# Optimization experiments

Measured on AMD Instinct MI355X. Metric: run time of the kernel, lower is better.

Reference implementation:

```python
import jax, jax.numpy as jnp
from jax import lax
import numpy as np

B, C, O, NF, H, W = 4, 64, 64, 64, 128, 128
DK = 3
K = DK * DK
PAD = DK // 2


def setup_inputs() -> dict:
    key = jax.random.key(0)
    k0, k1, k2, k3 = jax.random.split(key, 4)
    inputs = jax.random.normal(k0, (B, C, H, W), jnp.float32)
    feat = jax.random.normal(k1, (B, NF, H, W), jnp.float32)
    # small offset-conv weights keep learned offsets in a realistic sub-pixel range
    om_w = jax.random.normal(k2, (C * 3 * K, NF, 3, 3), jnp.float32) * 0.02
    om_b = jnp.zeros((C * 3 * K,), jnp.float32)
    dc_w = jax.random.normal(k3, (O, C, DK, DK), jnp.float32) * (1.0 / np.sqrt(C * K))
    dc_b = jnp.zeros((O,), jnp.float32)
    return dict(inputs=inputs, feat=feat, om_w=om_w, om_b=om_b, dc_w=dc_w, dc_b=dc_b)


def _gather(img, y, x):
    # img: [B,C,H,W]; y,x: int32 [B,C,K,H,W]; zero outside bounds
    valid = (y >= 0) & (y < H) & (x >= 0) & (x < W)
    yc = jnp.clip(y, 0, H - 1)
    xc = jnp.clip(x, 0, W - 1)
    idx = (yc * W + xc).reshape(B, C, K, H * W)
    flat = img.reshape(B, C, 1, H * W)
    v = jnp.take_along_axis(flat, idx, axis=3).reshape(B, C, K, H, W)
    return jnp.where(valid, v, 0.0)


def _forward(inputs, feat, om_w, om_b, dc_w, dc_b):
    # offset/mask conv: nf -> in_nc*3*K, 3x3, pad 1
    off_msk = lax.conv_general_dilated(
        feat, om_w, (1, 1), ((1, 1), (1, 1)),
        dimension_numbers=('NCHW', 'OIHW', 'NCHW')) + om_b[None, :, None, None]
    # offsets interleaved (y,x) per kernel tap per deformable group (= channel)
    off = off_msk[:, :C * 2 * K].reshape(B, C, K, 2, H, W)
    msk = jax.nn.sigmoid(off_msk[:, C * 2 * K:]).reshape(B, C, K, H, W)

    ky = (jnp.arange(K) // DK - PAD).astype(jnp.float32)  # [K]
    kx = (jnp.arange(K) % DK - PAD).astype(jnp.float32)
    hg = jnp.arange(H, dtype=jnp.float32)
    wg = jnp.arange(W, dtype=jnp.float32)
    py = hg[None, None, None, :, None] + ky[None, None, :, None, None] + off[:, :, :, 0]  # [B,C,K,H,W]
    px = wg[None, None, None, None, :] + kx[None, None, :, None, None] + off[:, :, :, 1]

    y0f = jnp.floor(py); x0f = jnp.floor(px)
    wy = py - y0f; wx = px - x0f
    y0 = y0f.astype(jnp.int32); x0 = x0f.astype(jnp.int32)
    y1 = y0 + 1; x1 = x0 + 1

    v00 = _gather(inputs, y0, x0)
    v01 = _gather(inputs, y0, x1)
    v10 = _gather(inputs, y1, x0)
    v11 = _gather(inputs, y1, x1)
    sampled = ((1 - wy) * (1 - wx) * v00 + (1 - wy) * wx * v01
               + wy * (1 - wx) * v10 + wy * wx * v11) * msk  # [B,C,K,H,W]

    out = jnp.einsum('bckhw,ock->bohw', sampled, dc_w.reshape(O, C, K))
    out = out + dc_b[None, :, None, None]
    return jax.nn.relu(out)


def reference(inputs, feat, om_w, om_b, dc_w, dc_b):
    return _forward(inputs, feat, om_w, om_b, dc_w, dc_b)
```

## Files before the change

### kernel.cpp

```cpp
#include <hip/hip_runtime.h>
#include <hip/hip_bf16.h>

typedef __bf16 bf16;
typedef __bf16 bf16x8 __attribute__((ext_vector_type(8)));
typedef __bf16 bf16x4 __attribute__((ext_vector_type(4)));
typedef float f32x4 __attribute__((ext_vector_type(4)));
typedef float f32x2 __attribute__((ext_vector_type(2)));
typedef float f32x2u __attribute__((ext_vector_type(2))) __attribute__((aligned(4)));
typedef int  i32x4 __attribute__((ext_vector_type(4)));

#define MFMA16(a, b, c) __builtin_amdgcn_mfma_f32_16x16x32_bf16((a), (b), (c), 0, 0, 0)

static constexpr size_t FEATS_OFF = 0;
static constexpr size_t OMW3_OFF  = 8388608;
static constexpr size_t DCW_OFF   = OMW3_OFF + 1990656;
static constexpr size_t SC_OFF    = DCW_OFF + 73728;
static constexpr size_t PAD_OFF   = SC_OFF + 9216;


__global__ void prep_featS(const float* __restrict__ feat, bf16* __restrict__ featS) {
    const int hh = blockIdx.x, b = blockIdx.y;
    __shared__ float t[64][129];
    for (int i = threadIdx.x; i < 64 * 32; i += 256) {
        int cf = i >> 5, q = i & 31;
        const float* src = feat + ((size_t)(b * 64 + cf) * 128 + hh) * 128 + q * 4;
        t[cf][q * 4 + 0] = src[0];
        t[cf][q * 4 + 1] = src[1];
        t[cf][q * 4 + 2] = src[2];
        t[cf][q * 4 + 3] = src[3];
    }
    __syncthreads();
    for (int i = threadIdx.x; i < 1024; i += 256) {
        int px = i >> 3, cfb = i & 7;
        int sb = cfb ^ (px & 7);
        bf16x8 v;
#pragma unroll
        for (int e = 0; e < 8; ++e) v[e] = (bf16)t[cfb * 8 + e][px];
        *(bf16x8*)(featS + ((size_t)((b * 128 + hh) * 128 + px) << 6) + sb * 8) = v;
    }
}

__global__ void prep_weights(const float* __restrict__ om_w, const float* __restrict__ om_b,
                             const float* __restrict__ dc_w,
                             bf16* __restrict__ omw3, bf16* __restrict__ dcw2p,
                             float* __restrict__ scf) {
    int i = blockIdx.x * 256 + threadIdx.x;
    if (i < 995328) {
        int e = i & 511, lane = e >> 3, j = e & 7;
        int q = i >> 9;
        int t = q % 3, q2 = q / 3, kk = q2 % 18, ct = q2 / 18;
        int ck = ct * 16 + (lane & 15);
        int kcol = kk * 32 + (lane >> 4) * 8 + j;
        int tap = kcol >> 6, cf = kcol & 63;
        int ch = (t < 2) ? (ck * 2 + t) : (1152 + ck);
        omw3[i] = (bf16)om_w[ch * 576 + cf * 9 + tap];
    }
    if (i < 36864) {
        int j = i & 7, lane = (i >> 3) & 63, ot = (i >> 9) & 3, win = i >> 11;
        int o = ot * 16 + (lane & 15);
        int ck = win * 32 + (lane >> 4) * 8 + j;
        dcw2p[i] = (bf16)dc_w[o * 576 + ck];
    }
    if (i < 576) {
        int ck = i;
        int c = ck / 9, kd = ck - 9 * c, kq = kd / 3, kx = kd - 3 * kq;
        int pr = ck >> 1, lo = ck & 1;
        scf[pr * 8 + 0 + lo] = om_b[ck * 2]     + (float)(kq + 2);
        scf[pr * 8 + 2 + lo] = om_b[ck * 2 + 1] + (float)(kx + 2);
        scf[pr * 8 + 4 + lo] = om_b[1152 + ck];
        scf[pr * 8 + 6 + lo] = __uint_as_float((unsigned)(c * 17956));
    }
}

__global__ void prep_pad(const float* __restrict__ inputs, float* __restrict__ pad) {
    int yy = blockIdx.x, bc = blockIdx.y, xx = threadIdx.x;
    if (xx >= 134) return;
    float v = 0.f;
    if (yy >= 3 && yy <= 130 && xx >= 3 && xx <= 130)
        v = inputs[(size_t)bc * 16384 + (yy - 3) * 128 + (xx - 3)];
    pad[((size_t)bc * 134 + yy) * 134 + xx] = v;
}


__global__ void __launch_bounds__(256, 4)
deform_fused(const float* __restrict__ pad,
             const bf16* __restrict__ featS,
             const bf16* __restrict__ omw3,
             const bf16* __restrict__ dcw2p,
             const f32x4* __restrict__ sconst,
             const float* __restrict__ dcb,
             float* __restrict__ out)
{
    const int bid = blockIdx.x;
    const int P0 = (bid & 1) << 6;
    const int h = (bid >> 1) & 127;
    const int b = bid >> 8;
    const int tid = threadIdx.x;
    const int lane = tid & 63;
    const int wid_s = __builtin_amdgcn_readfirstlane(tid >> 6);
    const int l15 = lane & 15, g = lane >> 4;

    __shared__ __align__(16) unsigned char smem[25344 + 8192];
    char* featB = (char*)smem;
    char* sampB = (char*)smem + 25344;

    for (int i = tid; i < 6336; i += 256) ((unsigned*)featB)[i] = 0u;
    __syncthreads();
    {
        const int s0 = (P0 == 0) ? 0 : 63;
        const int q0 = (P0 == 0) ? 1 : 0;
        for (int i = tid; i < 1560; i += 256) {
            int ky = i / 520, rem = i - ky * 520, row = rem >> 3, c = rem & 7;
            int hh = h - 1 + ky;
            if ((unsigned)hh < 128u) {
                const char* src = (const char*)featS
                    + (((size_t)(b * 128 + hh) * 128 + s0 + row) << 7) + c * 16;
                *(i32x4*)(featB + ((ky * 66 + q0 + row) << 7) + c * 16) = *(const i32x4*)src;
            }
        }
    }
    __syncthreads();

    int fb[18];
#pragma unroll
    for (int kk = 0; kk < 18; ++kk) {
        const int tap = kk >> 1;
        const int kyp = tap / 3, kxp = tap - 3 * kyp;
        const int q = l15 + kxp;
        fb[kk] = (kyp * 66 + q) * 128 + ((((kk & 1) * 4 + g) ^ ((q + 7) & 7)) << 4);
    }

    f32x4 acc2[4];
#pragma unroll
    for (int u = 0; u < 4; ++u) acc2[u] = (f32x4){0.f, 0.f, 0.f, 0.f};

    const bf16* omw3_l = omw3 + lane * 8;
    const bf16* dcw_l  = dcw2p + lane * 8;
    const float* padb0 = pad + (size_t)b * 64 * 17956;
    const f32x2 hb2 = {(float)h, (float)h};
    const f32x2 fx2 = {(float)(P0 + l15), (float)(P0 + l15)};
    const int g4 = g * 4;

#pragma unroll 1
    for (int blk = 0; blk < 9; ++blk) {
        f32x4 acc1[3][4];
#pragma unroll
        for (int t = 0; t < 3; ++t)
#pragma unroll
            for (int nf = 0; nf < 4; ++nf) acc1[t][nf] = (f32x4){0.f, 0.f, 0.f, 0.f};

        const int abase = (blk * 4 + wid_s) * 27648;

#pragma unroll
        for (int kk = 0; kk < 18; ++kk) {
            bf16x8 a0 = *(const bf16x8*)(omw3_l + abase + ((kk * 3 + 0) << 9));
            bf16x8 a1 = *(const bf16x8*)(omw3_l + abase + ((kk * 3 + 1) << 9));
            bf16x8 a2 = *(const bf16x8*)(omw3_l + abase + ((kk * 3 + 2) << 9));
            bf16x8 bfr[4];
#pragma unroll
            for (int nf = 0; nf < 4; ++nf)
                bfr[nf] = *(const bf16x8*)(featB + fb[kk] + nf * 2048);
            __builtin_amdgcn_s_setprio(1);
#pragma unroll
            for (int nf = 0; nf < 4; ++nf) {
                acc1[0][nf] = MFMA16(a0, bfr[nf], acc1[0][nf]);
                acc1[1][nf] = MFMA16(a1, bfr[nf], acc1[1][nf]);
                acc1[2][nf] = MFMA16(a2, bfr[nf], acc1[2][nf]);
            }
            __builtin_amdgcn_s_setprio(0);
        }

        bf16x8 aK0 = *(const bf16x8*)(dcw_l + ((blk * 8 + wid_s) << 9));
        bf16x8 aK1 = *(const bf16x8*)(dcw_l + ((blk * 8 + 4 + wid_s) << 9));

        const f32x4* scB = sconst + (blk * 64 + wid_s * 16);
        f32x4 e0A = scB[g4 + 0], e1A = scB[g4 + 1];
        f32x4 e0B = scB[g4 + 2], e1B = scB[g4 + 3];
        f32x2 yb[2], xb[2], mb[2];
        unsigned co[2][2];
        yb[0] = f32x2{e0A.x, e0A.y} + hb2;
        xb[0] = f32x2{e0A.z, e0A.w} + fx2;
        mb[0] = f32x2{e1A.x, e1A.y};
        co[0][0] = __float_as_uint(e1A.z); co[0][1] = __float_as_uint(e1A.w);
        yb[1] = f32x2{e0B.x, e0B.y} + hb2;
        xb[1] = f32x2{e0B.z, e0B.w} + fx2;
        mb[1] = f32x2{e1B.x, e1B.y};
        co[1][0] = __float_as_uint(e1B.z); co[1][1] = __float_as_uint(e1B.w);

#pragma unroll
        for (int nf = 0; nf < 4; ++nf) {
            float s[4];
#pragma unroll
            for (int pi = 0; pi < 2; ++pi) {
                f32x2 py = f32x2{acc1[0][nf][2 * pi], acc1[0][nf][2 * pi + 1]} + yb[pi];
                f32x2 px = f32x2{acc1[1][nf][2 * pi], acc1[1][nf][2 * pi + 1]} + xb[pi];
                f32x2 lg = f32x2{acc1[2][nf][2 * pi], acc1[2][nf][2 * pi + 1]} + mb[pi];
#pragma unroll
                for (int e = 0; e < 2; ++e) {
                    float pyc = __builtin_amdgcn_fmed3f(py[e], 0.5f, 132.5f);
                    float pxc = __builtin_amdgcn_fmed3f(px[e], 0.5f, 132.5f);
                    int y0 = (int)pyc, x0 = (int)pxc;
                    float wy = __builtin_amdgcn_fractf(pyc);
                    float wx = __builtin_amdgcn_fractf(pxc);
                    unsigned off = co[pi][e] + (unsigned)(y0 * 134 + x0);
                    f32x2u t0 = *(const f32x2u*)(padb0 + off);
                    f32x2u t1 = *(const f32x2u*)(padb0 + off + 134);
                    float top = t0.x + wx * (t0.y - t0.x);
                    float bot = t1.x + wx * (t1.y - t1.x);
                    float bil = top + wy * (bot - top);
                    float mk = __builtin_amdgcn_rcpf(1.f + __expf(-lg[e]));
                    s[2 * pi + e] = bil * mk;
                }
            }
            bf16x4 pk4 = {(bf16)s[0], (bf16)s[1], (bf16)s[2], (bf16)s[3]};
            *(bf16x4*)(sampB + (nf * 16 + l15) * 128
                       + (((wid_s * 4 + g) ^ ((l15 & 7) << 1)) << 3)) = pk4;
            xb[0] += 16.f; xb[1] += 16.f;
        }
        __syncthreads();

        const int rb_swz = (g ^ (l15 & 7)) << 4;
        __builtin_amdgcn_s_setprio(1);
#pragma unroll
        for (int u = 0; u < 4; ++u) {
            const int rb = (u * 16 + l15) * 128 + rb_swz;
            bf16x8 b0 = *(const bf16x8*)(sampB + rb);
            bf16x8 b1 = *(const bf16x8*)(sampB + (rb ^ 64));
            acc2[u] = MFMA16(aK0, b0, acc2[u]);
            acc2[u] = MFMA16(aK1, b1, acc2[u]);
        }
        __builtin_amdgcn_s_setprio(0);
        __syncthreads();
    }

    float bias[4];
#pragma unroll
    for (int r = 0; r < 4; ++r) bias[r] = dcb[wid_s * 16 + g * 4 + r];
#pragma unroll
    for (int u = 0; u < 4; ++u)
#pragma unroll
        for (int r = 0; r < 4; ++r) {
            int o = wid_s * 16 + g * 4 + r;
            out[((size_t)(b * 64 + o) * 128 + h) * 128 + P0 + u * 16 + l15]
                = fmaxf(acc2[u][r] + bias[r], 0.f);
        }
}

extern "C" void kernel_launch(void* const* d_in, const int* in_sizes, int n_in,
                              void* d_out, int out_size, void* d_ws, size_t ws_size,
                              hipStream_t stream) {
    const float* inputs = (const float*)d_in[0];
    const float* feat   = (const float*)d_in[1];
    const float* om_w   = (const float*)d_in[2];
    const float* om_b   = (const float*)d_in[3];
    const float* dc_w   = (const float*)d_in[4];
    const float* dc_b   = (const float*)d_in[5];
    float* out = (float*)d_out;

    char* ws = (char*)d_ws;
    bf16*  featS  = (bf16*)(ws + FEATS_OFF);
    bf16*  omw3   = (bf16*)(ws + OMW3_OFF);
    bf16*  dcw2p  = (bf16*)(ws + DCW_OFF);
    float* scf    = (float*)(ws + SC_OFF);
    float* pad    = (float*)(ws + PAD_OFF);

    prep_featS<<<dim3(128, 4), 256, 0, stream>>>(feat, featS);
    prep_weights<<<(995328 + 255) / 256, 256, 0, stream>>>(om_w, om_b, dc_w, omw3, dcw2p, scf);
    prep_pad<<<dim3(134, 256), 256, 0, stream>>>(inputs, pad);

    deform_fused<<<1024, 256, 0, stream>>>(pad, featS, omw3, dcw2p,
                                           (const f32x4*)scf, dc_b, out);
}
```

Measured before the change: 177.2 us.

## Switch fused deform kernel to 32x32x16 MFMA with register-resident samples

```diff
diff --git a/kernel.cpp b/kernel.cpp
--- a/kernel.cpp
+++ b/kernel.cpp
@@ -3,17 +3,16 @@
 
 typedef __bf16 bf16;
 typedef __bf16 bf16x8 __attribute__((ext_vector_type(8)));
-typedef __bf16 bf16x4 __attribute__((ext_vector_type(4)));
 typedef float f32x4 __attribute__((ext_vector_type(4)));
-typedef float f32x2 __attribute__((ext_vector_type(2)));
+typedef float f32x16 __attribute__((ext_vector_type(16)));
 typedef float f32x2u __attribute__((ext_vector_type(2))) __attribute__((aligned(4)));
 typedef int  i32x4 __attribute__((ext_vector_type(4)));
 
-#define MFMA16(a, b, c) __builtin_amdgcn_mfma_f32_16x16x32_bf16((a), (b), (c), 0, 0, 0)
+#define MFMA32(a, b, c) __builtin_amdgcn_mfma_f32_32x32x16_bf16((a), (b), (c), 0, 0, 0)
 
 static constexpr size_t FEATS_OFF = 0;
-static constexpr size_t OMW3_OFF  = 8388608;
-static constexpr size_t DCW_OFF   = OMW3_OFF + 1990656;
+static constexpr size_t OMW_OFF   = 8388608;
+static constexpr size_t DCW_OFF   = OMW_OFF + 1990656;
 static constexpr size_t SC_OFF    = DCW_OFF + 73728;
 static constexpr size_t PAD_OFF   = SC_OFF + 9216;
 
@@ -42,33 +41,40 @@
 
 __global__ void prep_weights(const float* __restrict__ om_w, const float* __restrict__ om_b,
                              const float* __restrict__ dc_w,
-                             bf16* __restrict__ omw3, bf16* __restrict__ dcw2p,
+                             bf16* __restrict__ omw32, bf16* __restrict__ dcw32,
                              float* __restrict__ scf) {
     int i = blockIdx.x * 256 + threadIdx.x;
     if (i < 995328) {
-        int e = i & 511, lane = e >> 3, j = e & 7;
-        int q = i >> 9;
-        int t = q % 3, q2 = q / 3, kk = q2 % 18, ct = q2 / 18;
-        int ck = ct * 16 + (lane & 15);
-        int kcol = kk * 32 + (lane >> 4) * 8 + j;
+        int j = i & 7, lane = (i >> 3) & 63;
+        int rest = i >> 9;
+        int s = rest % 36, rest2 = rest / 36;
+        int mt = rest2 % 6, blk = rest2 / 6;
+        int t = mt >> 1, ckh = mt & 1;
+        int ck = blk * 64 + ckh * 32 + (lane & 31);
+        int kcol = s * 16 + (lane >> 5) * 8 + j;
         int tap = kcol >> 6, cf = kcol & 63;
         int ch = (t < 2) ? (ck * 2 + t) : (1152 + ck);
-        omw3[i] = (bf16)om_w[ch * 576 + cf * 9 + tap];
+        omw32[i] = (bf16)om_w[ch * 576 + cf * 9 + tap];
     }
     if (i < 36864) {
-        int j = i & 7, lane = (i >> 3) & 63, ot = (i >> 9) & 3, win = i >> 11;
-        int o = ot * 16 + (lane & 15);
-        int ck = win * 32 + (lane >> 4) * 8 + j;
-        dcw2p[i] = (bf16)dc_w[o * 576 + ck];
-    }
-    if (i < 576) {
-        int ck = i;
+        int j = i & 7, lane = (i >> 3) & 63;
+        int rest = i >> 9;
+        int ot = rest & 1, ki = (rest >> 1) & 1, ckh = (rest >> 2) & 1, blk = rest >> 3;
+        int o = ot * 32 + (lane & 31);
+        int ck = blk * 64 + ckh * 32 + ki * 16 + (j & 3) + 8 * (j >> 2) + 4 * (lane >> 5);
+        dcw32[i] = (bf16)dc_w[o * 576 + ck];
+    }
+    if (i < 2304) {
+        int e = i & 3, vi = i >> 2;
+        int f = vi & 3, g = (vi >> 2) & 3, hi = (vi >> 4) & 1, ckh = (vi >> 5) & 1, blk = vi >> 6;
+        int ck = blk * 64 + ckh * 32 + 8 * g + 4 * hi + e;
         int c = ck / 9, kd = ck - 9 * c, kq = kd / 3, kx = kd - 3 * kq;
-        int pr = ck >> 1, lo = ck & 1;
-        scf[pr * 8 + 0 + lo] = om_b[ck * 2]     + (float)(kq + 2);
-        scf[pr * 8 + 2 + lo] = om_b[ck * 2 + 1] + (float)(kx + 2);
-        scf[pr * 8 + 4 + lo] = om_b[1152 + ck];
-        scf[pr * 8 + 6 + lo] = __uint_as_float((unsigned)(c * 17956));
+        float v;
+        if (f == 0)      v = om_b[2 * ck] + (float)(kq + 2);
+        else if (f == 1) v = om_b[2 * ck + 1] + (float)(kx + 2);
+        else if (f == 2) v = om_b[1152 + ck];
+        else             v = __uint_as_float((unsigned)(c * 17956));
+        scf[i] = v;
     }
 }
 
@@ -82,11 +88,11 @@
 }
 
 
-__global__ void __launch_bounds__(256, 4)
+__global__ void __launch_bounds__(256, 3)
 deform_fused(const float* __restrict__ pad,
              const bf16* __restrict__ featS,
-             const bf16* __restrict__ omw3,
-             const bf16* __restrict__ dcw2p,
+             const bf16* __restrict__ omw32,
+             const bf16* __restrict__ dcw32,
              const f32x4* __restrict__ sconst,
              const float* __restrict__ dcb,
              float* __restrict__ out)
@@ -98,11 +104,11 @@
     const int tid = threadIdx.x;
     const int lane = tid & 63;
     const int wid_s = __builtin_amdgcn_readfirstlane(tid >> 6);
-    const int l15 = lane & 15, g = lane >> 4;
-
-    __shared__ __align__(16) unsigned char smem[25344 + 8192];
+    const int ckh = wid_s & 1, nt = wid_s >> 1;
+    const int l31 = lane & 31, hi = lane >> 5;
+
+    __shared__ __align__(16) unsigned char smem[25344];
     char* featB = (char*)smem;
-    char* sampB = (char*)smem + 25344;
 
     for (int i = tid; i < 6336; i += 256) ((unsigned*)featB)[i] = 0u;
     __syncthreads();
@@ -121,129 +127,114 @@
     }
     __syncthreads();
 
-    int fb[18];
-#pragma unroll
-    for (int kk = 0; kk < 18; ++kk) {
-        const int tap = kk >> 1;
+    int base9[9];
+#pragma unroll
+    for (int tap = 0; tap < 9; ++tap) {
         const int kyp = tap / 3, kxp = tap - 3 * kyp;
-        const int q = l15 + kxp;
-        fb[kk] = (kyp * 66 + q) * 128 + ((((kk & 1) * 4 + g) ^ ((q + 7) & 7)) << 4);
-    }
-
-    f32x4 acc2[4];
-#pragma unroll
-    for (int u = 0; u < 4; ++u) acc2[u] = (f32x4){0.f, 0.f, 0.f, 0.f};
-
-    const bf16* omw3_l = omw3 + lane * 8;
-    const bf16* dcw_l  = dcw2p + lane * 8;
+        const int q = nt * 32 + l31 + kxp;
+        base9[tap] = (kyp * 66 + q) * 128 + ((hi ^ ((q + 7) & 7)) << 4);
+    }
+
+    f32x16 acc2a = {}, acc2b = {};
+
+    const bf16* omw_l = omw32 + lane * 8;
+    const bf16* dcw_l = dcw32 + lane * 8;
     const float* padb0 = pad + (size_t)b * 64 * 17956;
-    const f32x2 hb2 = {(float)h, (float)h};
-    const f32x2 fx2 = {(float)(P0 + l15), (float)(P0 + l15)};
-    const int g4 = g * 4;
+    const float hf = (float)h;
+    const float fx = (float)(P0 + nt * 32 + l31);
 
 #pragma unroll 1
     for (int blk = 0; blk < 9; ++blk) {
-        f32x4 acc1[3][4];
-#pragma unroll
-        for (int t = 0; t < 3; ++t)
-#pragma unroll
-            for (int nf = 0; nf < 4; ++nf) acc1[t][nf] = (f32x4){0.f, 0.f, 0.f, 0.f};
-
-        const int abase = (blk * 4 + wid_s) * 27648;
-
-#pragma unroll
-        for (int kk = 0; kk < 18; ++kk) {
-            bf16x8 a0 = *(const bf16x8*)(omw3_l + abase + ((kk * 3 + 0) << 9));
-            bf16x8 a1 = *(const bf16x8*)(omw3_l + abase + ((kk * 3 + 1) << 9));
-            bf16x8 a2 = *(const bf16x8*)(omw3_l + abase + ((kk * 3 + 2) << 9));
-            bf16x8 bfr[4];
-#pragma unroll
-            for (int nf = 0; nf < 4; ++nf)
-                bfr[nf] = *(const bf16x8*)(featB + fb[kk] + nf * 2048);
+        f32x16 c0 = {}, c1 = {}, c2 = {};
+        const size_t ab = ((size_t)(blk * 216 + ckh * 36)) * 512;
+
+#pragma unroll
+        for (int s = 0; s < 36; ++s) {
+            bf16x8 a0 = *(const bf16x8*)(omw_l + ab + (size_t)s * 512);
+            bf16x8 a1 = *(const bf16x8*)(omw_l + ab + (size_t)(s + 72) * 512);
+            bf16x8 a2 = *(const bf16x8*)(omw_l + ab + (size_t)(s + 144) * 512);
+            bf16x8 bfr = *(const bf16x8*)(featB + (base9[s >> 2] ^ ((s & 3) << 5)));
             __builtin_amdgcn_s_setprio(1);
-#pragma unroll
-            for (int nf = 0; nf < 4; ++nf) {
-                acc1[0][nf] = MFMA16(a0, bfr[nf], acc1[0][nf]);
-                acc1[1][nf] = MFMA16(a1, bfr[nf], acc1[1][nf]);
-                acc1[2][nf] = MFMA16(a2, bfr[nf], acc1[2][nf]);
-            }
+            c0 = MFMA32(a0, bfr, c0);
+            c1 = MFMA32(a1, bfr, c1);
+            c2 = MFMA32(a2, bfr, c2);
             __builtin_amdgcn_s_setprio(0);
         }
 
-        bf16x8 aK0 = *(const bf16x8*)(dcw_l + ((blk * 8 + wid_s) << 9));
-        bf16x8 aK1 = *(const bf16x8*)(dcw_l + ((blk * 8 + 4 + wid_s) << 9));
-
-        const f32x4* scB = sconst + (blk * 64 + wid_s * 16);
-        f32x4 e0A = scB[g4 + 0], e1A = scB[g4 + 1];
-        f32x4 e0B = scB[g4 + 2], e1B = scB[g4 + 3];
-        f32x2 yb[2], xb[2], mb[2];
-        unsigned co[2][2];
-        yb[0] = f32x2{e0A.x, e0A.y} + hb2;
-        xb[0] = f32x2{e0A.z, e0A.w} + fx2;
-        mb[0] = f32x2{e1A.x, e1A.y};
-        co[0][0] = __float_as_uint(e1A.z); co[0][1] = __float_as_uint(e1A.w);
-        yb[1] = f32x2{e0B.x, e0B.y} + hb2;
-        xb[1] = f32x2{e0B.z, e0B.w} + fx2;
-        mb[1] = f32x2{e1B.x, e1B.y};
-        co[1][0] = __float_as_uint(e1B.z); co[1][1] = __float_as_uint(e1B.w);
-
-#pragma unroll
-        for (int nf = 0; nf < 4; ++nf) {
-            float s[4];
-#pragma unroll
-            for (int pi = 0; pi < 2; ++pi) {
-                f32x2 py = f32x2{acc1[0][nf][2 * pi], acc1[0][nf][2 * pi + 1]} + yb[pi];
-                f32x2 px = f32x2{acc1[1][nf][2 * pi], acc1[1][nf][2 * pi + 1]} + xb[pi];
-                f32x2 lg = f32x2{acc1[2][nf][2 * pi], acc1[2][nf][2 * pi + 1]} + mb[pi];
-#pragma unroll
-                for (int e = 0; e < 2; ++e) {
-                    float pyc = __builtin_amdgcn_fmed3f(py[e], 0.5f, 132.5f);
-                    float pxc = __builtin_amdgcn_fmed3f(px[e], 0.5f, 132.5f);
-                    int y0 = (int)pyc, x0 = (int)pxc;
-                    float wy = __builtin_amdgcn_fractf(pyc);
-                    float wx = __builtin_amdgcn_fractf(pxc);
-                    unsigned off = co[pi][e] + (unsigned)(y0 * 134 + x0);
-                    f32x2u t0 = *(const f32x2u*)(padb0 + off);
-                    f32x2u t1 = *(const f32x2u*)(padb0 + off + 134);
-                    float top = t0.x + wx * (t0.y - t0.x);
-                    float bot = t1.x + wx * (t1.y - t1.x);
-                    float bil = top + wy * (bot - top);
-                    float mk = __builtin_amdgcn_rcpf(1.f + __expf(-lg[e]));
-                    s[2 * pi + e] = bil * mk;
-                }
-            }
-            bf16x4 pk4 = {(bf16)s[0], (bf16)s[1], (bf16)s[2], (bf16)s[3]};
-            *(bf16x4*)(sampB + (nf * 16 + l15) * 128
-                       + (((wid_s * 4 + g) ^ ((l15 & 7) << 1)) << 3)) = pk4;
-            xb[0] += 16.f; xb[1] += 16.f;
-        }
-        __syncthreads();
-
-        const int rb_swz = (g ^ (l15 & 7)) << 4;
+        bf16x8 B0 = {}, B1 = {};
+        const f32x4* scg = sconst + ((size_t)((blk * 2 + ckh) * 2 + hi)) * 16;
+#pragma unroll
+        for (int g = 0; g < 4; ++g) {
+            f32x4 yb = scg[g * 4 + 0];
+            f32x4 xb = scg[g * 4 + 1];
+            f32x4 mb = scg[g * 4 + 2];
+            f32x4 co = scg[g * 4 + 3];
+#pragma unroll
+            for (int e = 0; e < 4; ++e) {
+                const int r = g * 4 + e;
+                float py = c0[r] + yb[e] + hf;
+                float px = c1[r] + xb[e] + fx;
+                float lg = c2[r] + mb[e];
+                float pyc = __builtin_amdgcn_fmed3f(py, 0.5f, 132.5f);
+                float pxc = __builtin_amdgcn_fmed3f(px, 0.5f, 132.5f);
+                int y0 = (int)pyc, x0 = (int)pxc;
+                float wy = __builtin_amdgcn_fractf(pyc);
+                float wx = __builtin_amdgcn_fractf(pxc);
+                unsigned off = __float_as_uint(co[e]) + (unsigned)(y0 * 134 + x0);
+                f32x2u t0 = *(const f32x2u*)(padb0 + off);
+                f32x2u t1 = *(const f32x2u*)(padb0 + off + 134);
+                float top = t0.x + wx * (t0.y - t0.x);
+                float bot = t1.x + wx * (t1.y - t1.x);
+                float bil = top + wy * (bot - top);
+                float mk = __builtin_amdgcn_rcpf(1.f + __expf(-lg));
+                float sv = bil * mk;
+                if (r < 8) B0[r] = (bf16)sv;
+                else       B1[r - 8] = (bf16)sv;
+            }
+        }
+
+        const bf16* dk = dcw_l + ((size_t)((blk * 4 + ckh * 2)) << 10);
+        bf16x8 aK00 = *(const bf16x8*)(dk);
+        bf16x8 aK01 = *(const bf16x8*)(dk + 512);
+        bf16x8 aK10 = *(const bf16x8*)(dk + 1024);
+        bf16x8 aK11 = *(const bf16x8*)(dk + 1536);
         __builtin_amdgcn_s_setprio(1);
-#pragma unroll
-        for (int u = 0; u < 4; ++u) {
-            const int rb = (u * 16 + l15) * 128 + rb_swz;
-            bf16x8 b0 = *(const bf16x8*)(sampB + rb);
-            bf16x8 b1 = *(const bf16x8*)(sampB + (rb ^ 64));
-            acc2[u] = MFMA16(aK0, b0, acc2[u]);
-            acc2[u] = MFMA16(aK1, b1, acc2[u]);
-        }
+        acc2a = MFMA32(aK00, B0, acc2a);
+        acc2b = MFMA32(aK01, B0, acc2b);
+        acc2a = MFMA32(aK10, B1, acc2a);
+        acc2b = MFMA32(aK11, B1, acc2b);
         __builtin_amdgcn_s_setprio(0);
-        __syncthreads();
-    }
-
-    float bias[4];
-#pragma unroll
-    for (int r = 0; r < 4; ++r) bias[r] = dcb[wid_s * 16 + g * 4 + r];
-#pragma unroll
-    for (int u = 0; u < 4; ++u)
-#pragma unroll
-        for (int r = 0; r < 4; ++r) {
-            int o = wid_s * 16 + g * 4 + r;
-            out[((size_t)(b * 64 + o) * 128 + h) * 128 + P0 + u * 16 + l15]
-                = fmaxf(acc2[u][r] + bias[r], 0.f);
-        }
+    }
+
+    __syncthreads();
+    float* red = (float*)smem;
+    if (ckh) {
+#pragma unroll
+        for (int r = 0; r < 16; ++r) {
+            int o0 = (r & 3) + 8 * (r >> 2) + 4 * hi;
+            red[(nt * 64 + o0) * 32 + l31] = acc2a[r];
+            red[(nt * 64 + 32 + o0) * 32 + l31] = acc2b[r];
+        }
+    }
+    __syncthreads();
+    if (!ckh) {
+#pragma unroll
+        for (int r = 0; r < 16; ++r) {
+            int o0 = (r & 3) + 8 * (r >> 2) + 4 * hi;
+            {
+                int o = o0;
+                float v = red[(nt * 64 + o) * 32 + l31] + acc2a[r] + dcb[o];
+                out[((size_t)(b * 64 + o) * 128 + h) * 128 + P0 + nt * 32 + l31]
+                    = fmaxf(v, 0.f);
+            }
+            {
+                int o = 32 + o0;
+                float v = red[(nt * 64 + o) * 32 + l31] + acc2b[r] + dcb[o];
+                out[((size_t)(b * 64 + o) * 128 + h) * 128 + P0 + nt * 32 + l31]
+                    = fmaxf(v, 0.f);
+            }
+        }
+    }
 }
 
 extern "C" void kernel_launch(void* const* d_in, const int* in_sizes, int n_in,
@@ -258,16 +249,16 @@
     float* out = (float*)d_out;
 
     char* ws = (char*)d_ws;
-    bf16*  featS  = (bf16*)(ws + FEATS_OFF);
-    bf16*  omw3   = (bf16*)(ws + OMW3_OFF);
-    bf16*  dcw2p  = (bf16*)(ws + DCW_OFF);
-    float* scf    = (float*)(ws + SC_OFF);
-    float* pad    = (float*)(ws + PAD_OFF);
+    bf16*  featS = (bf16*)(ws + FEATS_OFF);
+    bf16*  omw32 = (bf16*)(ws + OMW_OFF);
+    bf16*  dcw32 = (bf16*)(ws + DCW_OFF);
+    float* scf   = (float*)(ws + SC_OFF);
+    float* pad   = (float*)(ws + PAD_OFF);
 
     prep_featS<<<dim3(128, 4), 256, 0, stream>>>(feat, featS);
-    prep_weights<<<(995328 + 255) / 256, 256, 0, stream>>>(om_w, om_b, dc_w, omw3, dcw2p, scf);
+    prep_weights<<<(995328 + 255) / 256, 256, 0, stream>>>(om_w, om_b, dc_w, omw32, dcw32, scf);
     prep_pad<<<dim3(134, 256), 256, 0, stream>>>(inputs, pad);
 
-    deform_fused<<<1024, 256, 0, stream>>>(pad, featS, omw3, dcw2p,
+    deform_fused<<<1024, 256, 0, stream>>>(pad, featS, omw32, dcw32,
                                            (const f32x4*)scf, dc_b, out);
 }
```

Measured after the change: 362.0 us. 104% more time.
